# Kernel optimization log

Hardware: AMD Instinct MI355X
Metric: run time of the kernel (lower is better)

## Reference

```python
import jax, jax.numpy as jnp
import numpy as np

HIDDEN = 1024
B, S = 32, 2048
MASKED_BIAS = -10000.0


def setup_inputs() -> dict:
    key = jax.random.key(0)
    ks = jax.random.split(key, 10)
    scale = 1.0 / np.sqrt(HIDDEN)
    inp = {
        "h": jax.random.normal(ks[0], (B, HIDDEN), jnp.float32),
        "K": jax.random.normal(ks[1], (B, S, HIDDEN), jnp.float32),
        "cov": jax.random.uniform(ks[2], (B, S), jnp.float32),
        "mask": jax.random.bernoulli(ks[3], 0.1, (B, S)).astype(jnp.float32),
        # parameters (PyTorch Linear: y = x @ W.T + b)
        "W_h": jax.random.uniform(ks[4], (HIDDEN, HIDDEN), jnp.float32, -scale, scale),
        "b_h": jnp.zeros((HIDDEN,), jnp.float32),
        "W_K": jax.random.uniform(ks[5], (HIDDEN, HIDDEN), jnp.float32, -scale, scale),
        "b_K": jnp.zeros((HIDDEN,), jnp.float32),
        "W_cov": jax.random.uniform(ks[6], (HIDDEN, 1), jnp.float32, -1.0, 1.0),
        "b_cov": jnp.zeros((HIDDEN,), jnp.float32),
        "W_v": jax.random.uniform(ks[7], (1, HIDDEN), jnp.float32, -scale, scale),
        "b_v": jnp.zeros((1,), jnp.float32),
    }
    return inp


def reference(h, K, cov, mask, W_h, b_h, W_K, b_K, W_cov, b_cov, W_v, b_v):
    # h_l: (B, 1, H); K_l: (B, S, H); c_l: (B, S, H)
    h_l = (h @ W_h.T + b_h)[:, None, :]
    K_l = jnp.einsum("bsh,gh->bsg", K, W_K) + b_K
    c_l = cov[:, :, None] * W_cov[:, 0] + b_cov  # linear_cov on scalar cov
    t = jnp.tanh(h_l + K_l + c_l)                 # (B, S, H)
    e = jnp.einsum("bsh,h->bs", t, W_v[0]) + b_v[0]
    e = e + mask * MASKED_BIAS
    a = jax.nn.softmax(e, axis=-1)                # (B, S)
    out = jnp.einsum("bs,bsh->bh", a, K)          # context vector
    cov_new = cov + a
    return (out, a, cov_new)
```

## Files before the change

kernel.cpp:

```cpp
#include <hip/hip_runtime.h>
#include <hip/hip_bf16.h>

#define HIDDEN 1024
#define B_SZ 32
#define S_SZ 2048
#define M_TOT (B_SZ * S_SZ)
#define MASKED_BIAS -10000.0f

using bf16   = __bf16;
using bf16x4 = __attribute__((ext_vector_type(4))) __bf16;
using bf16x8 = __attribute__((ext_vector_type(8))) __bf16;
using f32x4  = __attribute__((ext_vector_type(4))) float;

__device__ __forceinline__ float tanh_fast(float x) {
    float xc = fminf(fmaxf(x, -15.f), 15.f);
    float e2 = __expf(2.f * xc);
    return (e2 - 1.f) * __frcp_rn(e2 + 1.f);
}

__global__ __launch_bounds__(256) void k_wconv(
    const float* __restrict__ W, bf16* __restrict__ out)
{
    int i = blockIdx.x * 256 + threadIdx.x;
    const float4* p = (const float4*)W + (size_t)i * 2;
    float4 a = p[0], b = p[1];
    bf16x8 v = { (bf16)a.x, (bf16)a.y, (bf16)a.z, (bf16)a.w,
                 (bf16)b.x, (bf16)b.y, (bf16)b.z, (bf16)b.w };
    *(bf16x8*)(out + (size_t)i * 8) = v;
}

__global__ __launch_bounds__(256) void k_kconv(
    const float* __restrict__ K, bf16* __restrict__ out)
{
    size_t i = (size_t)blockIdx.x * 256 + threadIdx.x;
    const float4* p = (const float4*)K + i * 2;
    float4 a = p[0], b = p[1];
    bf16x8 v = { (bf16)a.x, (bf16)a.y, (bf16)a.z, (bf16)a.w,
                 (bf16)b.x, (bf16)b.y, (bf16)b.z, (bf16)b.w };
    *(bf16x8*)(out + i * 8) = v;
}

__global__ __launch_bounds__(256) void k_hlplus(
    const float* __restrict__ h, const float* __restrict__ W_h,
    const float* __restrict__ b_h, const float* __restrict__ b_K,
    const float* __restrict__ b_cov, float* __restrict__ hl_plus)
{
    int wid  = blockIdx.x * 4 + (threadIdx.x >> 6);
    int lane = threadIdx.x & 63;
    int b = wid & 31;
    int g = wid >> 5;
    const float4* hv = (const float4*)(h + b * HIDDEN);
    const float4* wv = (const float4*)(W_h + g * HIDDEN);
    float acc = 0.f;
#pragma unroll
    for (int i = 0; i < 4; ++i) {
        float4 a = hv[i * 64 + lane];
        float4 w = wv[i * 64 + lane];
        acc += a.x * w.x + a.y * w.y + a.z * w.z + a.w * w.w;
    }
#pragma unroll
    for (int off = 32; off; off >>= 1) acc += __shfl_xor(acc, off);
    if (lane == 0)
        hl_plus[b * HIDDEN + g] = acc + b_h[g] + b_K[g] + b_cov[g];
}

#define NT_N 8

__global__ __launch_bounds__(256, 4) void k_fusedA(
    const bf16*  __restrict__ Kbf,
    const bf16*  __restrict__ Bbf,
    const float* __restrict__ hl_plus,
    const float* __restrict__ W_cov,
    const float* __restrict__ cov,
    const float* __restrict__ W_v,
    float* __restrict__ e_part)
{
    __shared__ __align__(16) bf16 As[2][128][32];
    __shared__ __align__(16) bf16 Bs[2][128][32];
    __shared__ float e_buf[128][2];

    const int tid = threadIdx.x;
    const int bid = blockIdx.x;
    const int lid = (bid & 7) * 512 + (bid >> 3);
    const int mt  = lid >> 3;
    const int nt  = lid & 7;
    const int row0 = mt * 128;
    const int col0 = nt * 128;

    const int w    = tid >> 6;
    const int lane = tid & 63;
    const int wm   = w >> 1;
    const int wn   = w & 1;
    const int lr   = lane & 15;
    const int kb   = lane >> 4;
    const int colA = (kb ^ ((lr >> 1) & 3)) * 8;

    const int srow = lane >> 2;
    const int gch  = (lane & 3) ^ ((lane >> 3) & 3);
    const bf16* Abase = Kbf + (size_t)(row0 + w * 16 + srow) * HIDDEN + gch * 8;
    const bf16* Bbase = Bbf + (size_t)(col0 + w * 16 + srow) * HIDDEN + gch * 8;

    f32x4 acc[4][4] = {};

#define STAGE(KT, BUF)                                                    \
    __builtin_amdgcn_global_load_lds(                                     \
        (const __attribute__((address_space(1))) void*)(Abase + (KT) * 32),\
        (__attribute__((address_space(3))) void*)&As[BUF][w * 16][0],     \
        16, 0, 0);                                                        \
    __builtin_amdgcn_global_load_lds(                                     \
        (const __attribute__((address_space(1))) void*)                   \
            (Abase + (size_t)64 * HIDDEN + (KT) * 32),                    \
        (__attribute__((address_space(3))) void*)&As[BUF][64 + w * 16][0],\
        16, 0, 0);                                                        \
    __builtin_amdgcn_global_load_lds(                                     \
        (const __attribute__((address_space(1))) void*)(Bbase + (KT) * 32),\
        (__attribute__((address_space(3))) void*)&Bs[BUF][w * 16][0],     \
        16, 0, 0);                                                        \
    __builtin_amdgcn_global_load_lds(                                     \
        (const __attribute__((address_space(1))) void*)                   \
            (Bbase + (size_t)64 * HIDDEN + (KT) * 32),                    \
        (__attribute__((address_space(3))) void*)&Bs[BUF][64 + w * 16][0],\
        16, 0, 0);

#define TILE_COMPUTE(BUF)                                                 \
    {                                                                     \
        bf16x8 afr[4], bfr[4];                                            \
        _Pragma("unroll") for (int j = 0; j < 4; ++j)                     \
            afr[j] = *(const bf16x8*)                                     \
                &As[BUF][wm * 64 + j * 16 + lr][colA];                    \
        _Pragma("unroll") for (int n = 0; n < 4; ++n)                     \
            bfr[n] = *(const bf16x8*)&Bs[BUF][wn * 64 + n * 16 + lr][colA];\
        __builtin_amdgcn_s_setprio(1);                                    \
        _Pragma("unroll") for (int j = 0; j < 4; ++j)                     \
            _Pragma("unroll") for (int n = 0; n < 4; ++n)                 \
                acc[j][n] = __builtin_amdgcn_mfma_f32_16x16x32_bf16(      \
                    afr[j], bfr[n], acc[j][n], 0, 0, 0);                  \
        __builtin_amdgcn_s_setprio(0);                                    \
    }

    STAGE(0, 0)
    __syncthreads();

    for (int i = 0; i < 15; ++i) {
        const int t = i * 2;
        STAGE(t + 1, 1)
        TILE_COMPUTE(0)
        __syncthreads();
        STAGE(t + 2, 0)
        TILE_COMPUTE(1)
        __syncthreads();
    }
    STAGE(31, 1)
    TILE_COMPUTE(0)
    __syncthreads();
    TILE_COMPUTE(1)

    const int bidx = row0 >> 11;
    float hlv[4], wcv[4], wvv[4];
#pragma unroll
    for (int n = 0; n < 4; ++n) {
        int g = col0 + wn * 64 + n * 16 + lr;
        hlv[n] = hl_plus[bidx * HIDDEN + g];
        wcv[n] = W_cov[g];
        wvv[n] = W_v[g];
    }
#pragma unroll
    for (int j = 0; j < 4; ++j) {
#pragma unroll
        for (int i = 0; i < 4; ++i) {
            int rloc = wm * 64 + j * 16 + kb * 4 + i;
            float cv = cov[row0 + rloc];
            float ep = 0.f;
#pragma unroll
            for (int n = 0; n < 4; ++n) {
                float arg = acc[j][n][i] + hlv[n] + cv * wcv[n];
                ep += tanh_fast(arg) * wvv[n];
            }
            ep += __shfl_xor(ep, 1);
            ep += __shfl_xor(ep, 2);
            ep += __shfl_xor(ep, 4);
            ep += __shfl_xor(ep, 8);
            if (lr == 0) e_buf[rloc][wn] = ep;
        }
    }
    __syncthreads();
    if (tid < 128)
        e_part[(size_t)nt * M_TOT + row0 + tid] = e_buf[tid][0] + e_buf[tid][1];

#undef STAGE
#undef TILE_COMPUTE
}

__global__ __launch_bounds__(256) void k_softmax(
    const float* __restrict__ e_part, const float* __restrict__ mask,
    const float* __restrict__ cov, const float* __restrict__ b_v,
    float* __restrict__ a_out, float* __restrict__ cov_out)
{
    __shared__ float red[8];
    int b = blockIdx.x, tid = threadIdx.x;
    float bv = b_v[0];
    float ev[8];
    float mx = -1e30f;
#pragma unroll
    for (int j = 0; j < 8; ++j) {
        int s = j * 256 + tid;
        int idx = b * S_SZ + s;
        float e = bv;
#pragma unroll
        for (int p = 0; p < 8; ++p) e += e_part[(size_t)p * M_TOT + idx];
        e += mask[idx] * MASKED_BIAS;
        ev[j] = e;
        mx = fmaxf(mx, e);
    }
#pragma unroll
    for (int off = 32; off; off >>= 1) mx = fmaxf(mx, __shfl_xor(mx, off));
    if ((tid & 63) == 0) red[tid >> 6] = mx;
    __syncthreads();
    mx = fmaxf(fmaxf(red[0], red[1]), fmaxf(red[2], red[3]));
    float sum = 0.f;
#pragma unroll
    for (int j = 0; j < 8; ++j) { ev[j] = __expf(ev[j] - mx); sum += ev[j]; }
#pragma unroll
    for (int off = 32; off; off >>= 1) sum += __shfl_xor(sum, off);
    if ((tid & 63) == 0) red[4 + (tid >> 6)] = sum;
    __syncthreads();
    sum = red[4] + red[5] + red[6] + red[7];
    float inv = 1.f / sum;
#pragma unroll
    for (int j = 0; j < 8; ++j) {
        int idx = b * S_SZ + j * 256 + tid;
        float a = ev[j] * inv;
        a_out[idx]   = a;
        cov_out[idx] = cov[idx] + a;
    }
}

__global__ __launch_bounds__(256) void k_ctx_part_bf(
    const bf16* __restrict__ Kbf, const float* __restrict__ a_out,
    float* __restrict__ part_out)
{
    int sc = blockIdx.x;
    int b  = blockIdx.y;
    int tid = threadIdx.x;
    const bf16* Kb = Kbf + ((size_t)b * S_SZ + sc * 128) * HIDDEN;
    const float* ab = a_out + b * S_SZ + sc * 128;
    float4 acc = {0.f, 0.f, 0.f, 0.f};
#pragma unroll 4
    for (int s = 0; s < 128; ++s) {
        float av = ab[s];
        bf16x4 kv = *(const bf16x4*)(Kb + (size_t)s * HIDDEN + tid * 4);
        acc.x += av * (float)kv[0];
        acc.y += av * (float)kv[1];
        acc.z += av * (float)kv[2];
        acc.w += av * (float)kv[3];
    }
    ((float4*)part_out)[((size_t)b * 16 + sc) * 256 + tid] = acc;
}

__global__ __launch_bounds__(256) void k_ctx_reduce(
    const float* __restrict__ part_out, float* __restrict__ out, int nc)
{
    int b = blockIdx.x, tid = threadIdx.x;
    float4 acc = {0.f, 0.f, 0.f, 0.f};
    for (int sc = 0; sc < nc; ++sc) {
        float4 v = ((const float4*)part_out)[((size_t)b * nc + sc) * 256 + tid];
        acc.x += v.x; acc.y += v.y; acc.z += v.z; acc.w += v.w;
    }
    ((float4*)out)[b * 256 + tid] = acc;
}

extern "C" void kernel_launch(void* const* d_in, const int* in_sizes, int n_in,
                              void* d_out, int out_size, void* d_ws, size_t ws_size,
                              hipStream_t stream)
{
    const float* h     = (const float*)d_in[0];
    const float* Kin   = (const float*)d_in[1];
    const float* cov   = (const float*)d_in[2];
    const float* mask  = (const float*)d_in[3];
    const float* W_h   = (const float*)d_in[4];
    const float* b_h   = (const float*)d_in[5];
    const float* W_K   = (const float*)d_in[6];
    const float* b_K   = (const float*)d_in[7];
    const float* W_cov = (const float*)d_in[8];
    const float* b_cov = (const float*)d_in[9];
    const float* W_v   = (const float*)d_in[10];
    const float* b_v   = (const float*)d_in[11];

    float* out_ctx = (float*)d_out;
    float* a_out   = out_ctx + B_SZ * HIDDEN;
    float* cov_out = a_out + M_TOT;

    float* ws       = (float*)d_ws;
    float* hl_plus  = ws;
    float* e_part   = ws + 32768;
    float* part_out = e_part;
    bf16*  Bbf      = (bf16*)(e_part + 8 * M_TOT);
    bf16*  Kbf      = (bf16*)((char*)Bbf + (size_t)HIDDEN * HIDDEN * sizeof(bf16));

    k_wconv<<<512, 256, 0, stream>>>(W_K, Bbf);
    k_hlplus<<<8192, 256, 0, stream>>>(h, W_h, b_h, b_K, b_cov, hl_plus);
    k_kconv<<<(M_TOT * HIDDEN / 8) / 256, 256, 0, stream>>>(Kin, Kbf);
    k_fusedA<<<512 * NT_N, 256, 0, stream>>>(
        Kbf, Bbf, hl_plus, W_cov, cov, W_v, e_part);
    k_softmax<<<B_SZ, 256, 0, stream>>>(e_part, mask, cov, b_v, a_out, cov_out);
    dim3 g4(16, B_SZ);
    k_ctx_part_bf<<<g4, 256, 0, stream>>>(Kbf, a_out, part_out);
    k_ctx_reduce<<<B_SZ, 256, 0, stream>>>(part_out, out_ctx, 16);
}
```

Before: 289.4 us.

## Fuse K fp32-to-bf16 conversion into GEMM tile loads, drop separate kconv pass

```diff
diff --git a/kernel.cpp b/kernel.cpp
--- a/kernel.cpp
+++ b/kernel.cpp
@@ -27,17 +27,6 @@
     bf16x8 v = { (bf16)a.x, (bf16)a.y, (bf16)a.z, (bf16)a.w,
                  (bf16)b.x, (bf16)b.y, (bf16)b.z, (bf16)b.w };
     *(bf16x8*)(out + (size_t)i * 8) = v;
-}
-
-__global__ __launch_bounds__(256) void k_kconv(
-    const float* __restrict__ K, bf16* __restrict__ out)
-{
-    size_t i = (size_t)blockIdx.x * 256 + threadIdx.x;
-    const float4* p = (const float4*)K + i * 2;
-    float4 a = p[0], b = p[1];
-    bf16x8 v = { (bf16)a.x, (bf16)a.y, (bf16)a.z, (bf16)a.w,
-                 (bf16)b.x, (bf16)b.y, (bf16)b.z, (bf16)b.w };
-    *(bf16x8*)(out + i * 8) = v;
 }
 
 __global__ __launch_bounds__(256) void k_hlplus(
@@ -66,8 +55,8 @@
 
 #define NT_N 8
 
-__global__ __launch_bounds__(256, 4) void k_fusedA(
-    const bf16*  __restrict__ Kbf,
+__global__ __launch_bounds__(256, 4) void k_fusedF(
+    const float* __restrict__ Kin,
     const bf16*  __restrict__ Bbf,
     const float* __restrict__ hl_plus,
     const float* __restrict__ W_cov,
@@ -75,8 +64,8 @@
     const float* __restrict__ W_v,
     float* __restrict__ e_part)
 {
-    __shared__ __align__(16) bf16 As[2][128][32];
-    __shared__ __align__(16) bf16 Bs[2][128][32];
+    __shared__ __align__(16) float As[2][128][32];
+    __shared__ __align__(16) bf16  Bs[2][128][32];
     __shared__ float e_buf[128][2];
 
     const int tid = threadIdx.x;
@@ -93,43 +82,47 @@
     const int wn   = w & 1;
     const int lr   = lane & 15;
     const int kb   = lane >> 4;
-    const int colA = (kb ^ ((lr >> 1) & 3)) * 8;
-
-    const int srow = lane >> 2;
-    const int gch  = (lane & 3) ^ ((lane >> 3) & 3);
-    const bf16* Abase = Kbf + (size_t)(row0 + w * 16 + srow) * HIDDEN + gch * 8;
-    const bf16* Bbase = Bbf + (size_t)(col0 + w * 16 + srow) * HIDDEN + gch * 8;
+    const int colB = (kb ^ ((lr >> 1) & 3)) * 8;
+    const int cA0  = ((2 * kb)     ^ (lr & 7)) * 4;
+    const int cA1  = ((2 * kb + 1) ^ (lr & 7)) * 4;
+
+    const int arow = lane >> 3;
+    const int agch = (lane & 7) ^ arow;
+    const float* Abase =
+        Kin + (size_t)(row0 + w * 32 + arow) * HIDDEN + agch * 4;
+    const int brow = lane >> 2;
+    const int bgch = (lane & 3) ^ ((lane >> 3) & 3);
+    const bf16* Bbase =
+        Bbf + (size_t)(col0 + w * 16 + brow) * HIDDEN + bgch * 8;
 
     f32x4 acc[4][4] = {};
 
+#define GL(SRC, DST) __builtin_amdgcn_global_load_lds(                    \
+        (const __attribute__((address_space(1))) void*)(SRC),             \
+        (__attribute__((address_space(3))) void*)(DST), 16, 0, 0);
+
 #define STAGE(KT, BUF)                                                    \
-    __builtin_amdgcn_global_load_lds(                                     \
-        (const __attribute__((address_space(1))) void*)(Abase + (KT) * 32),\
-        (__attribute__((address_space(3))) void*)&As[BUF][w * 16][0],     \
-        16, 0, 0);                                                        \
-    __builtin_amdgcn_global_load_lds(                                     \
-        (const __attribute__((address_space(1))) void*)                   \
-            (Abase + (size_t)64 * HIDDEN + (KT) * 32),                    \
-        (__attribute__((address_space(3))) void*)&As[BUF][64 + w * 16][0],\
-        16, 0, 0);                                                        \
-    __builtin_amdgcn_global_load_lds(                                     \
-        (const __attribute__((address_space(1))) void*)(Bbase + (KT) * 32),\
-        (__attribute__((address_space(3))) void*)&Bs[BUF][w * 16][0],     \
-        16, 0, 0);                                                        \
-    __builtin_amdgcn_global_load_lds(                                     \
-        (const __attribute__((address_space(1))) void*)                   \
-            (Bbase + (size_t)64 * HIDDEN + (KT) * 32),                    \
-        (__attribute__((address_space(3))) void*)&Bs[BUF][64 + w * 16][0],\
-        16, 0, 0);
+    GL(Abase + (KT) * 32,                        &As[BUF][w * 32][0])     \
+    GL(Abase + (size_t)8  * HIDDEN + (KT) * 32,  &As[BUF][w * 32 +  8][0])\
+    GL(Abase + (size_t)16 * HIDDEN + (KT) * 32,  &As[BUF][w * 32 + 16][0])\
+    GL(Abase + (size_t)24 * HIDDEN + (KT) * 32,  &As[BUF][w * 32 + 24][0])\
+    GL(Bbase + (KT) * 32,                        &Bs[BUF][w * 16][0])     \
+    GL(Bbase + (size_t)64 * HIDDEN + (KT) * 32,  &Bs[BUF][64 + w * 16][0])
 
 #define TILE_COMPUTE(BUF)                                                 \
     {                                                                     \
         bf16x8 afr[4], bfr[4];                                            \
-        _Pragma("unroll") for (int j = 0; j < 4; ++j)                     \
-            afr[j] = *(const bf16x8*)                                     \
-                &As[BUF][wm * 64 + j * 16 + lr][colA];                    \
+        _Pragma("unroll") for (int j = 0; j < 4; ++j) {                   \
+            const float* rp = &As[BUF][wm * 64 + j * 16 + lr][0];         \
+            f32x4 a0 = *(const f32x4*)(rp + cA0);                         \
+            f32x4 a1 = *(const f32x4*)(rp + cA1);                         \
+            bf16x8 t = { (bf16)a0[0], (bf16)a0[1], (bf16)a0[2],           \
+                         (bf16)a0[3], (bf16)a1[0], (bf16)a1[1],           \
+                         (bf16)a1[2], (bf16)a1[3] };                      \
+            afr[j] = t;                                                   \
+        }                                                                 \
         _Pragma("unroll") for (int n = 0; n < 4; ++n)                     \
-            bfr[n] = *(const bf16x8*)&Bs[BUF][wn * 64 + n * 16 + lr][colA];\
+            bfr[n] = *(const bf16x8*)&Bs[BUF][wn * 64 + n * 16 + lr][colB];\
         __builtin_amdgcn_s_setprio(1);                                    \
         _Pragma("unroll") for (int j = 0; j < 4; ++j)                     \
             _Pragma("unroll") for (int n = 0; n < 4; ++n)                 \
@@ -187,6 +180,7 @@
     if (tid < 128)
         e_part[(size_t)nt * M_TOT + row0 + tid] = e_buf[tid][0] + e_buf[tid][1];
 
+#undef GL
 #undef STAGE
 #undef TILE_COMPUTE
 }
@@ -235,26 +229,24 @@
     }
 }
 
-__global__ __launch_bounds__(256) void k_ctx_part_bf(
-    const bf16* __restrict__ Kbf, const float* __restrict__ a_out,
+__global__ __launch_bounds__(256) void k_ctx_part(
+    const float* __restrict__ Kin, const float* __restrict__ a_out,
     float* __restrict__ part_out)
 {
     int sc = blockIdx.x;
     int b  = blockIdx.y;
     int tid = threadIdx.x;
-    const bf16* Kb = Kbf + ((size_t)b * S_SZ + sc * 128) * HIDDEN;
-    const float* ab = a_out + b * S_SZ + sc * 128;
+    const float4* Kb = (const float4*)(Kin + ((size_t)b * S_SZ + sc * 256) * HIDDEN);
+    const float*  ab = a_out + b * S_SZ + sc * 256;
     float4 acc = {0.f, 0.f, 0.f, 0.f};
 #pragma unroll 4
-    for (int s = 0; s < 128; ++s) {
+    for (int s = 0; s < 256; ++s) {
         float av = ab[s];
-        bf16x4 kv = *(const bf16x4*)(Kb + (size_t)s * HIDDEN + tid * 4);
-        acc.x += av * (float)kv[0];
-        acc.y += av * (float)kv[1];
-        acc.z += av * (float)kv[2];
-        acc.w += av * (float)kv[3];
-    }
-    ((float4*)part_out)[((size_t)b * 16 + sc) * 256 + tid] = acc;
+        float4 kv = Kb[(size_t)s * 256 + tid];
+        acc.x += av * kv.x; acc.y += av * kv.y;
+        acc.z += av * kv.z; acc.w += av * kv.w;
+    }
+    ((float4*)part_out)[((size_t)b * 8 + sc) * 256 + tid] = acc;
 }
 
 __global__ __launch_bounds__(256) void k_ctx_reduce(
@@ -295,15 +287,13 @@
     float* e_part   = ws + 32768;
     float* part_out = e_part;
     bf16*  Bbf      = (bf16*)(e_part + 8 * M_TOT);
-    bf16*  Kbf      = (bf16*)((char*)Bbf + (size_t)HIDDEN * HIDDEN * sizeof(bf16));
 
     k_wconv<<<512, 256, 0, stream>>>(W_K, Bbf);
     k_hlplus<<<8192, 256, 0, stream>>>(h, W_h, b_h, b_K, b_cov, hl_plus);
-    k_kconv<<<(M_TOT * HIDDEN / 8) / 256, 256, 0, stream>>>(Kin, Kbf);
-    k_fusedA<<<512 * NT_N, 256, 0, stream>>>(
-        Kbf, Bbf, hl_plus, W_cov, cov, W_v, e_part);
+    k_fusedF<<<512 * NT_N, 256, 0, stream>>>(
+        Kin, Bbf, hl_plus, W_cov, cov, W_v, e_part);
     k_softmax<<<B_SZ, 256, 0, stream>>>(e_part, mask, cov, b_v, a_out, cov_out);
-    dim3 g4(16, B_SZ);
-    k_ctx_part_bf<<<g4, 256, 0, stream>>>(Kbf, a_out, part_out);
-    k_ctx_reduce<<<B_SZ, 256, 0, stream>>>(part_out, out_ctx, 16);
-}
+    dim3 g4(8, B_SZ);
+    k_ctx_part<<<g4, 256, 0, stream>>>(Kin, a_out, part_out);
+    k_ctx_reduce<<<B_SZ, 256, 0, stream>>>(part_out, out_ctx, 8);
+}
```

After: 378.4 us. 30.7% more time.
